# Kernel optimization log

Measured on AMD Instinct MI355X. Metric: run time of the kernel, lower is better.

## Reference

```python
import jax, jax.numpy as jnp
import numpy as np

D_MODEL = 2048
BATCH, SEQ = 4, 8192
T_STEPS = 10


def setup_inputs() -> dict:
    key = jax.random.key(0)
    k1, k2, k3 = jax.random.split(key, 3)
    latent = jax.random.normal(k1, (BATCH, SEQ, D_MODEL), dtype=jnp.float32)
    W = jax.random.normal(k2, (3, D_MODEL), dtype=jnp.float32) * (1.0 / np.sqrt(D_MODEL))
    b = jnp.zeros((3,), dtype=jnp.float32)
    noise = jax.random.normal(k3, (BATCH, SEQ, 3), dtype=jnp.float32)
    return {"latent": latent, "W": W, "b": b, "noise": noise, "diffusion_steps": T_STEPS}


def reference(latent, W, b, noise, diffusion_steps):
    # coords = Linear(d_model, 3)(latent)
    coords = jnp.einsum("bsd,cd->bsc", latent, W) + b  # [B, S, 3]
    # x_{k+1} = alpha * x_k + (1 - alpha) * coords, alpha = (t+1)/T, t = T-1..0.
    # diffusion_steps is a static Python int, so this unrolls to T fused FMAs.
    x = noise
    T = diffusion_steps
    for t in reversed(range(T)):
        alpha = (t + 1) / T
        x = alpha * x + (1.0 - alpha) * coords
    return x
```

## Files before the change

kernel.cpp:

```cpp
#include <hip/hip_runtime.h>

#define D_MODEL 2048
#define D4 (D_MODEL / 4)

__global__ __launch_bounds__(256) void diff_coord_kernel(
    const float* __restrict__ latent,
    const float* __restrict__ W,
    const float* __restrict__ b,
    const float* __restrict__ noise,
    const int*   __restrict__ tsteps,
    float*       __restrict__ out,
    int nrows)
{
    __shared__ float4 wlds[3][D4];

    const float4* W4 = reinterpret_cast<const float4*>(W);
    for (int i = threadIdx.x; i < 3 * D4; i += 256) {
        wlds[i / D4][i % D4] = W4[i];
    }
    __syncthreads();

    const int wid  = threadIdx.x >> 6;
    const int lane = threadIdx.x & 63;
    const int T    = tsteps[0];

    for (int row = blockIdx.x * 4 + wid; row < nrows; row += gridDim.x * 4) {
        const float4* lat4 =
            reinterpret_cast<const float4*>(latent) + (size_t)row * D4;

        float a0 = 0.0f, a1 = 0.0f, a2 = 0.0f;
        #pragma unroll
        for (int k = 0; k < D4 / 64; ++k) {
            const int j = k * 64 + lane;
            const float4 x  = lat4[j];
            const float4 w0 = wlds[0][j];
            const float4 w1 = wlds[1][j];
            const float4 w2 = wlds[2][j];
            a0 += x.x * w0.x; a0 += x.y * w0.y; a0 += x.z * w0.z; a0 += x.w * w0.w;
            a1 += x.x * w1.x; a1 += x.y * w1.y; a1 += x.z * w1.z; a1 += x.w * w1.w;
            a2 += x.x * w2.x; a2 += x.y * w2.y; a2 += x.z * w2.z; a2 += x.w * w2.w;
        }

        #pragma unroll
        for (int off = 32; off >= 1; off >>= 1) {
            a0 += __shfl_xor(a0, off);
            a1 += __shfl_xor(a1, off);
            a2 += __shfl_xor(a2, off);
        }

        if (lane < 3) {
            const float c = (lane == 0 ? a0 : (lane == 1 ? a1 : a2)) + b[lane];
            float x = noise[(size_t)row * 3 + lane];
            for (int t = T - 1; t >= 0; --t) {
                const float alpha = (float)(t + 1) / (float)T;
                x = alpha * x + (1.0f - alpha) * c;
            }
            out[(size_t)row * 3 + lane] = x;
        }
    }
}

extern "C" void kernel_launch(void* const* d_in, const int* in_sizes, int n_in,
                              void* d_out, int out_size, void* d_ws, size_t ws_size,
                              hipStream_t stream) {
    const float* latent = (const float*)d_in[0];
    const float* W      = (const float*)d_in[1];
    const float* b      = (const float*)d_in[2];
    const float* noise  = (const float*)d_in[3];
    const int*   tsteps = (const int*)d_in[4];
    float* out = (float*)d_out;

    const int nrows = in_sizes[0] / D_MODEL;

    diff_coord_kernel<<<2048, 256, 0, stream>>>(latent, W, b, noise, tsteps,
                                                out, nrows);
}
```

Measured before the change: 49.25 us.

## Drop LDS weight staging, use nontemporal latent loads and closed-form diffusion

Weights are no longer staged in shared memory; each wave reads them straight from global memory, relying on cache hits, which removes the block-level sync and the LDS fill. Latent rows are read with nontemporal loads so the streamed data does not evict the weights from cache. The noise load is issued before the dot product, and the T-step recurrence becomes a closed form p*noise + q*c, with p computed once per thread as a product. The kernel is memory-bound, so the main effect should come from load behaviour. The risks are more global/L1 traffic for weights and a small change in floating-point rounding.

```diff
diff --git a/kernel.cpp b/kernel.cpp
--- a/kernel.cpp
+++ b/kernel.cpp
@@ -2,6 +2,8 @@
 
 #define D_MODEL 2048
 #define D4 (D_MODEL / 4)
+
+typedef float f32x4 __attribute__((ext_vector_type(4)));
 
 __global__ __launch_bounds__(256) void diff_coord_kernel(
     const float* __restrict__ latent,
@@ -12,33 +14,39 @@
     float*       __restrict__ out,
     int nrows)
 {
-    __shared__ float4 wlds[3][D4];
-
-    const float4* W4 = reinterpret_cast<const float4*>(W);
-    for (int i = threadIdx.x; i < 3 * D4; i += 256) {
-        wlds[i / D4][i % D4] = W4[i];
-    }
-    __syncthreads();
-
     const int wid  = threadIdx.x >> 6;
     const int lane = threadIdx.x & 63;
     const int T    = tsteps[0];
 
-    for (int row = blockIdx.x * 4 + wid; row < nrows; row += gridDim.x * 4) {
-        const float4* lat4 =
-            reinterpret_cast<const float4*>(latent) + (size_t)row * D4;
+    float p = 1.0f;
+    for (int t = 1; t <= T; ++t) p *= (float)t / (float)T;
+    const float q = 1.0f - p;
+
+    const float bias = (lane < 3) ? b[lane] : 0.0f;
+
+    const f32x4* W4 = reinterpret_cast<const f32x4*>(W);
+    const int nwaves = gridDim.x * 4;
+
+    for (int row = blockIdx.x * 4 + wid; row < nrows; row += nwaves) {
+        const float nz = (lane < 3) ? noise[(size_t)row * 3 + lane] : 0.0f;
+
+        const f32x4* lat4 =
+            reinterpret_cast<const f32x4*>(latent) + (size_t)row * D4;
 
         float a0 = 0.0f, a1 = 0.0f, a2 = 0.0f;
         #pragma unroll
-        for (int k = 0; k < D4 / 64; ++k) {
-            const int j = k * 64 + lane;
-            const float4 x  = lat4[j];
-            const float4 w0 = wlds[0][j];
-            const float4 w1 = wlds[1][j];
-            const float4 w2 = wlds[2][j];
-            a0 += x.x * w0.x; a0 += x.y * w0.y; a0 += x.z * w0.z; a0 += x.w * w0.w;
-            a1 += x.x * w1.x; a1 += x.y * w1.y; a1 += x.z * w1.z; a1 += x.w * w1.w;
-            a2 += x.x * w2.x; a2 += x.y * w2.y; a2 += x.z * w2.z; a2 += x.w * w2.w;
+        for (int kk = 0; kk < 2; ++kk) {
+            #pragma unroll
+            for (int k = 0; k < 4; ++k) {
+                const int j = kk * 256 + k * 64 + lane;
+                const f32x4 x  = __builtin_nontemporal_load(lat4 + j);
+                const f32x4 w0 = W4[j];
+                const f32x4 w1 = W4[D4 + j];
+                const f32x4 w2 = W4[2 * D4 + j];
+                a0 += x.x * w0.x + x.y * w0.y + x.z * w0.z + x.w * w0.w;
+                a1 += x.x * w1.x + x.y * w1.y + x.z * w1.z + x.w * w1.w;
+                a2 += x.x * w2.x + x.y * w2.y + x.z * w2.z + x.w * w2.w;
+            }
         }
 
         #pragma unroll
@@ -49,13 +57,8 @@
         }
 
         if (lane < 3) {
-            const float c = (lane == 0 ? a0 : (lane == 1 ? a1 : a2)) + b[lane];
-            float x = noise[(size_t)row * 3 + lane];
-            for (int t = T - 1; t >= 0; --t) {
-                const float alpha = (float)(t + 1) / (float)T;
-                x = alpha * x + (1.0f - alpha) * c;
-            }
-            out[(size_t)row * 3 + lane] = x;
+            const float c = (lane == 0 ? a0 : (lane == 1 ? a1 : a2)) + bias;
+            out[(size_t)row * 3 + lane] = p * nz + q * c;
         }
     }
 }
```

New measurement: 58.99 us. 19.8% more time.
